# Kernel optimization log

Hardware: AMD Instinct MI355X
Metric: run time of the kernel (lower is better)

## Reference

```python
import jax, jax.numpy as jnp
import numpy as np

EMB = 1024
HEADS = 16
HEAD_DIM = EMB // HEADS


def setup_inputs() -> dict:
    key = jax.random.key(0)
    ks = jax.random.split(key, 5)
    x = jax.random.normal(ks[0], (4, 2048, EMB), dtype=jnp.float32)
    # qkv Linear: weight [3*EMB, EMB] in torch; store transposed for x @ W
    Wqkv = jax.random.normal(ks[1], (EMB, 3 * EMB), dtype=jnp.float32) * (1.0 / np.sqrt(EMB))
    bqkv = jax.random.normal(ks[2], (3 * EMB,), dtype=jnp.float32) * 0.01
    Wout = jax.random.normal(ks[3], (EMB, EMB), dtype=jnp.float32) * (1.0 / np.sqrt(EMB))
    bout = jax.random.normal(ks[4], (EMB,), dtype=jnp.float32) * 0.01
    return {"x": x, "Wqkv": Wqkv, "bqkv": bqkv, "Wout": Wout, "bout": bout}


def reference(x, Wqkv, bqkv, Wout, bout):
    B, N, _ = x.shape
    qkv = x @ Wqkv + bqkv                              # [B, N, 3*EMB]
    qkv = qkv.reshape(B, N, 3, HEADS, HEAD_DIM)
    q, k, v = jnp.moveaxis(qkv, 2, 0)                  # each [B, N, H, D]
    q = jnp.swapaxes(q, 1, 2)                          # [B, H, N, D]
    k = jnp.swapaxes(k, 1, 2)
    v = jnp.swapaxes(v, 1, 2)
    scale = 1.0 / np.sqrt(HEAD_DIM).astype(np.float32)
    scores = jnp.einsum('bhqd,bhkd->bhqk', q, k) * scale
    attn = jax.nn.softmax(scores, axis=-1)             # dropout p=0 (eval)
    out = jnp.einsum('bhqk,bhkd->bhqd', attn, v)       # [B, H, N, D]
    out = jnp.swapaxes(out, 1, 2).reshape(B, N, EMB)
    return out @ Wout + bout
```

## Files before the change

kernel.cpp:

```cpp
#include <hip/hip_runtime.h>

#define SEQ   2048
#define EMBD  1024
#define HEADS 16
#define HDIM  64
#define MTOT  8192
#define LOG2E 1.44269504f

typedef __attribute__((ext_vector_type(8))) _Float16 half8;
typedef __attribute__((ext_vector_type(4))) _Float16 half4;
typedef __attribute__((ext_vector_type(2))) __fp16 fp16x2;
typedef __attribute__((ext_vector_type(4))) float f32x4;

__device__ __forceinline__ f32x4 mfma16(half8 a, half8 b, f32x4 c) {
  return __builtin_amdgcn_mfma_f32_16x16x32_f16(a, b, c, 0, 0, 0);
}

__device__ __forceinline__ void gload_lds16(const void* g, void* l) {
  __builtin_amdgcn_global_load_lds(
      (const __attribute__((address_space(1))) unsigned int*)g,
      (__attribute__((address_space(3))) unsigned int*)l, 16, 0, 0);
}

__global__ void k_cvt(const float* __restrict__ in, _Float16* __restrict__ out) {
  size_t i = (size_t)blockIdx.x * blockDim.x + threadIdx.x;
  const f32x4* in4 = (const f32x4*)in;
  f32x4 a = in4[2 * i], b = in4[2 * i + 1];
  half8 h;
  h[0] = (_Float16)a[0]; h[1] = (_Float16)a[1];
  h[2] = (_Float16)a[2]; h[3] = (_Float16)a[3];
  h[4] = (_Float16)b[0]; h[5] = (_Float16)b[1];
  h[6] = (_Float16)b[2]; h[7] = (_Float16)b[3];
  *(half8*)(out + i * 8) = h;
}

__global__ __launch_bounds__(256) void k_transpose(const float* __restrict__ in,
                                                   _Float16* __restrict__ out,
                                                   int R, int C) {
  __shared__ _Float16 tile[64][65];
  const int tid = threadIdx.x;
  const int r0 = blockIdx.y * 64, c0 = blockIdx.x * 64;
  const int tr = tid >> 6;
  const int tc = tid & 63;
  #pragma unroll
  for (int i = 0; i < 16; ++i) {
    const int r = i * 4 + tr;
    tile[r][tc] = (_Float16)in[(size_t)(r0 + r) * C + c0 + tc];
  }
  __syncthreads();
  #pragma unroll
  for (int i = 0; i < 16; ++i) {
    const int cc = i * 4 + tr;
    out[(size_t)(c0 + cc) * R + r0 + tc] = tile[tc][cc];
  }
}

template<int EPI>
__global__ __launch_bounds__(256) void k_gemm(
    const _Float16* __restrict__ A, const _Float16* __restrict__ Bt,
    const float* __restrict__ bias, float* __restrict__ outf,
    _Float16* __restrict__ q, _Float16* __restrict__ k, _Float16* __restrict__ vt)
{
  __shared__ _Float16 sm[2 * 128 * 64];
  _Float16* sA = sm;
  _Float16* sB = sm + 128 * 64;
  const int tid = threadIdx.x;
  const int l = tid & 63, g = l >> 4, c = l & 15;
  const int w = tid >> 6;
  const int wm = (w >> 1) * 64, wn = (w & 1) * 64;
  const int rowBase = blockIdx.y * 128;
  const int colBase = blockIdx.x * 128;

  f32x4 acc[4][4] = {};

  const _Float16* Ag = A + (size_t)(rowBase + (tid >> 3)) * 1024 + (tid & 7) * 8;
  const _Float16* Bg = Bt + (size_t)(colBase + (tid >> 3)) * 1024 + (tid & 7) * 8;
  _Float16* la = sA + tid * 8;
  _Float16* lb = sB + tid * 8;

  for (int kt = 0; kt < 16; ++kt) {
    const _Float16* ag = Ag + kt * 64;
    const _Float16* bg = Bg + kt * 64;
    #pragma unroll
    for (int i = 0; i < 4; ++i) {
      gload_lds16(ag + (size_t)i * 32 * 1024, la + i * 256 * 8);
      gload_lds16(bg + (size_t)i * 32 * 1024, lb + i * 256 * 8);
    }
    __syncthreads();
    #pragma unroll
    for (int kk = 0; kk < 2; ++kk) {
      half8 af[4], bf[4];
      #pragma unroll
      for (int t = 0; t < 4; ++t)
        af[t] = *(const half8*)(sA + (wm + t * 16 + c) * 64 + kk * 32 + g * 8);
      #pragma unroll
      for (int t = 0; t < 4; ++t)
        bf[t] = *(const half8*)(sB + (wn + t * 16 + c) * 64 + kk * 32 + g * 8);
      #pragma unroll
      for (int mt = 0; mt < 4; ++mt)
        #pragma unroll
        for (int nt = 0; nt < 4; ++nt)
          acc[mt][nt] = mfma16(af[mt], bf[nt], acc[mt][nt]);
    }
    __syncthreads();
  }

  #pragma unroll
  for (int mt = 0; mt < 4; ++mt) {
    #pragma unroll
    for (int nt = 0; nt < 4; ++nt) {
      const int col = colBase + wn + nt * 16 + c;
      const float bv = bias[col];
      #pragma unroll
      for (int r = 0; r < 4; ++r) {
        const int row = rowBase + wm + mt * 16 + g * 4 + r;
        const float val = acc[mt][nt][r] + bv;
        if constexpr (EPI == 0) {
          const int s = col >> 10, h = (col >> 6) & 15, d = col & 63;
          const int b = row >> 11, n = row & 2047;
          const int bh = b * HEADS + h;
          const _Float16 hv = (_Float16)val;
          if (s == 2)      vt[((size_t)bh * HDIM + d) * SEQ + n] = hv;
          else if (s == 1) k [((size_t)bh * SEQ + n) * HDIM + d] = hv;
          else             q [((size_t)bh * SEQ + n) * HDIM + d] = hv;
        } else {
          outf[(size_t)row * EMBD + col] = val;
        }
      }
    }
  }
}

__global__ __launch_bounds__(512) void k_attn(
    const _Float16* __restrict__ q, const _Float16* __restrict__ kg,
    const _Float16* __restrict__ vt, _Float16* __restrict__ aout)
{
  __shared__ _Float16 sm[(64 + 64 + 8 * 32) * 72];
  _Float16* Ks = sm;
  _Float16* Vs = sm + 64 * 72;
  const int tid = threadIdx.x;
  const int w = tid >> 6, l = tid & 63, g = l >> 4, c = l & 15;
  _Float16* Pw = sm + 2 * 64 * 72 + w * 32 * 72;

  const int orig = blockIdx.x;
  const int lb = (orig & 7) * 64 + (orig >> 3);
  const int bh = lb >> 3;
  const int n0 = (lb & 7) * 256 + w * 32;

  const _Float16* qb = q  + (size_t)bh * SEQ * HDIM;
  const _Float16* kb = kg + (size_t)bh * SEQ * HDIM;
  const _Float16* vb = vt + (size_t)bh * HDIM * SEQ;
  const int row0 = tid >> 3, cb = tid & 7;

  half8 aq[2][2];
  #pragma unroll
  for (int qt = 0; qt < 2; ++qt)
    #pragma unroll
    for (int kk = 0; kk < 2; ++kk) {
      half8 t = *(const half8*)(qb + (size_t)(n0 + qt * 16 + c) * HDIM + kk * 32 + g * 8);
      aq[qt][kk] = t * (_Float16)0.125f;
    }

  float m_[2] = {-1e30f, -1e30f};
  float l_[2] = {0.f, 0.f};
  f32x4 o[2][4] = {};

  half8 kr = *(const half8*)(kb + (size_t)tid * 8);
  half8 vr = *(const half8*)(vb + (size_t)row0 * SEQ + cb * 8);

  for (int kt = 0; kt < SEQ / 64; ++kt) {
    __syncthreads();
    *(half8*)(Ks + row0 * 72 + cb * 8) = kr;
    *(half8*)(Vs + row0 * 72 + cb * 8) = vr;
    if (kt + 1 < SEQ / 64) {
      kr = *(const half8*)(kb + (size_t)(kt + 1) * 64 * HDIM + (size_t)tid * 8);
      vr = *(const half8*)(vb + (size_t)row0 * SEQ + (kt + 1) * 64 + cb * 8);
    }
    __syncthreads();

    f32x4 s[4][2] = {};
    __builtin_amdgcn_s_setprio(1);
    #pragma unroll
    for (int kk = 0; kk < 2; ++kk) {
      #pragma unroll
      for (int kt4 = 0; kt4 < 4; ++kt4) {
        half8 ak = *(const half8*)(Ks + (kt4 * 16 + c) * 72 + kk * 32 + g * 8);
        s[kt4][0] = mfma16(ak, aq[0][kk], s[kt4][0]);
        s[kt4][1] = mfma16(ak, aq[1][kk], s[kt4][1]);
      }
    }
    __builtin_amdgcn_s_setprio(0);

    #pragma unroll
    for (int qf = 0; qf < 2; ++qf) {
      float mx = s[0][qf][0];
      #pragma unroll
      for (int kt4 = 0; kt4 < 4; ++kt4)
        #pragma unroll
        for (int r = 0; r < 4; ++r)
          mx = fmaxf(mx, s[kt4][qf][r]);

      if (__any(mx > m_[qf] + 8.0f)) {
        float fm = fmaxf(mx, __shfl_xor(mx, 16, 64));
        fm = fmaxf(fm, __shfl_xor(fm, 32, 64));
        const float mo = m_[qf];
        const float mn = fmaxf(mo, fm);
        const float cor = __builtin_amdgcn_exp2f((mo - mn) * LOG2E);
        m_[qf] = mn;
        l_[qf] *= cor;
        #pragma unroll
        for (int r = 0; r < 4; ++r) {
          const float corr = __shfl(cor, g * 4 + r, 64);
          #pragma unroll
          for (int dt = 0; dt < 4; ++dt)
            o[qf][dt][r] *= corr;
        }
      }
      const float mn = m_[qf];

      float rs = 0.f;
      _Float16* prow = Pw + (qf * 16 + c) * 72;
      #pragma unroll
      for (int kt4 = 0; kt4 < 4; ++kt4) {
        float p0 = __builtin_amdgcn_exp2f((s[kt4][qf][0] - mn) * LOG2E);
        float p1 = __builtin_amdgcn_exp2f((s[kt4][qf][1] - mn) * LOG2E);
        float p2 = __builtin_amdgcn_exp2f((s[kt4][qf][2] - mn) * LOG2E);
        float p3 = __builtin_amdgcn_exp2f((s[kt4][qf][3] - mn) * LOG2E);
        rs += (p0 + p1) + (p2 + p3);
        union { fp16x2 v2[2]; half4 v4; } u;
        u.v2[0] = __builtin_amdgcn_cvt_pkrtz(p0, p1);
        u.v2[1] = __builtin_amdgcn_cvt_pkrtz(p2, p3);
        *(half4*)(prow + kt4 * 16 + g * 4) = u.v4;
      }
      l_[qf] += rs;
    }

    __builtin_amdgcn_s_setprio(1);
    #pragma unroll
    for (int kk = 0; kk < 2; ++kk) {
      half8 ap0 = *(const half8*)(Pw + (0  + c) * 72 + kk * 32 + g * 8);
      half8 ap1 = *(const half8*)(Pw + (16 + c) * 72 + kk * 32 + g * 8);
      #pragma unroll
      for (int dt = 0; dt < 4; ++dt) {
        half8 bv = *(const half8*)(Vs + (dt * 16 + c) * 72 + kk * 32 + g * 8);
        o[0][dt] = mfma16(ap0, bv, o[0][dt]);
        o[1][dt] = mfma16(ap1, bv, o[1][dt]);
      }
    }
    __builtin_amdgcn_s_setprio(0);
  }

  const int b = bh >> 4, h = bh & 15;
  #pragma unroll
  for (int qt = 0; qt < 2; ++qt) {
    float lt = l_[qt];
    lt += __shfl_xor(lt, 16, 64);
    lt += __shfl_xor(lt, 32, 64);
    #pragma unroll
    for (int r = 0; r < 4; ++r) {
      const float lr = __shfl(lt, g * 4 + r, 64);
      const float rl = __builtin_amdgcn_rcpf(lr);
      const int n = n0 + qt * 16 + g * 4 + r;
      #pragma unroll
      for (int dt = 0; dt < 4; ++dt) {
        aout[((size_t)(b * SEQ + n)) * EMBD + h * HDIM + dt * 16 + c] =
            (_Float16)(o[qt][dt][r] * rl);
      }
    }
  }
}

extern "C" void kernel_launch(void* const* d_in, const int* in_sizes, int n_in,
                              void* d_out, int out_size, void* d_ws, size_t ws_size,
                              hipStream_t stream) {
  const float* x    = (const float*)d_in[0];
  const float* Wqkv = (const float*)d_in[1];
  const float* bqkv = (const float*)d_in[2];
  const float* Wout = (const float*)d_in[3];
  const float* bout = (const float*)d_in[4];
  float* out = (float*)d_out;

  _Float16* ws    = (_Float16*)d_ws;
  _Float16* xh    = ws;
  _Float16* wqkvt = xh + (size_t)MTOT * EMBD;
  _Float16* woutt = wqkvt + (size_t)3 * EMBD * EMBD;
  _Float16* qbuf  = woutt + (size_t)EMBD * EMBD;
  _Float16* kbuf  = qbuf + (size_t)MTOT * EMBD;
  _Float16* vtbuf = kbuf + (size_t)MTOT * EMBD;
  _Float16* aout  = xh;

  k_cvt<<<4096, 256, 0, stream>>>(x, xh);
  k_transpose<<<dim3(48, 16), 256, 0, stream>>>(Wqkv, wqkvt, 1024, 3072);
  k_transpose<<<dim3(16, 16), 256, 0, stream>>>(Wout, woutt, 1024, 1024);
  k_gemm<0><<<dim3(24, 64), 256, 0, stream>>>(xh, wqkvt, bqkv, nullptr,
                                              qbuf, kbuf, vtbuf);
  k_attn<<<512, 512, 0, stream>>>(qbuf, kbuf, vtbuf, aout);
  k_gemm<1><<<dim3(8, 64), 256, 0, stream>>>(aout, woutt, bout, out,
                                             nullptr, nullptr, nullptr);
}
```

Before: 242.1 us.

## Switch attention kernel to 32x32x16 MFMA with per-lane query row softmax

The attention kernel moves from 16x16x32 to 32x32x16 MFMA tiles, computing S^T so that each lane owns one query row. Row max and row sum then need only one cross-lane shuffle, and the per-row correction shuffles go away. The output is staged through LDS so each lane writes a full 16-byte vector to global memory, and launch bounds now request 4 blocks per CU with a padded P stride. The risk is higher register pressure from the 16-wide accumulators, which could spill or lower occupancy.

```diff
diff --git a/kernel.cpp b/kernel.cpp
--- a/kernel.cpp
+++ b/kernel.cpp
@@ -11,15 +11,25 @@
 typedef __attribute__((ext_vector_type(4))) _Float16 half4;
 typedef __attribute__((ext_vector_type(2))) __fp16 fp16x2;
 typedef __attribute__((ext_vector_type(4))) float f32x4;
+typedef __attribute__((ext_vector_type(16))) float f32x16;
 
 __device__ __forceinline__ f32x4 mfma16(half8 a, half8 b, f32x4 c) {
   return __builtin_amdgcn_mfma_f32_16x16x32_f16(a, b, c, 0, 0, 0);
+}
+__device__ __forceinline__ f32x16 mfma32(half8 a, half8 b, f32x16 c) {
+  return __builtin_amdgcn_mfma_f32_32x32x16_f16(a, b, c, 0, 0, 0);
 }
 
 __device__ __forceinline__ void gload_lds16(const void* g, void* l) {
   __builtin_amdgcn_global_load_lds(
       (const __attribute__((address_space(1))) unsigned int*)g,
       (__attribute__((address_space(3))) unsigned int*)l, 16, 0, 0);
+}
+
+__device__ __forceinline__ unsigned pk2(float a, float b) {
+  union { fp16x2 v; unsigned u; } t;
+  t.v = __builtin_amdgcn_cvt_pkrtz(a, b);
+  return t.u;
 }
 
 __global__ void k_cvt(const float* __restrict__ in, _Float16* __restrict__ out) {
@@ -131,16 +141,17 @@
   }
 }
 
-__global__ __launch_bounds__(512) void k_attn(
+__global__ __launch_bounds__(512, 4) void k_attn(
     const _Float16* __restrict__ q, const _Float16* __restrict__ kg,
     const _Float16* __restrict__ vt, _Float16* __restrict__ aout)
 {
-  __shared__ _Float16 sm[(64 + 64 + 8 * 32) * 72];
+  __shared__ _Float16 sm[64 * 72 * 2 + 8 * 32 * 76];
   _Float16* Ks = sm;
   _Float16* Vs = sm + 64 * 72;
   const int tid = threadIdx.x;
-  const int w = tid >> 6, l = tid & 63, g = l >> 4, c = l & 15;
-  _Float16* Pw = sm + 2 * 64 * 72 + w * 32 * 72;
+  const int w = tid >> 6, l = tid & 63;
+  const int q32 = l & 31, hi = l >> 5;
+  _Float16* Pw = sm + 2 * 64 * 72 + w * 32 * 76;
 
   const int orig = blockIdx.x;
   const int lb = (orig & 7) * 64 + (orig >> 3);
@@ -152,18 +163,15 @@
   const _Float16* vb = vt + (size_t)bh * HDIM * SEQ;
   const int row0 = tid >> 3, cb = tid & 7;
 
-  half8 aq[2][2];
-  #pragma unroll
-  for (int qt = 0; qt < 2; ++qt)
-    #pragma unroll
-    for (int kk = 0; kk < 2; ++kk) {
-      half8 t = *(const half8*)(qb + (size_t)(n0 + qt * 16 + c) * HDIM + kk * 32 + g * 8);
-      aq[qt][kk] = t * (_Float16)0.125f;
-    }
-
-  float m_[2] = {-1e30f, -1e30f};
-  float l_[2] = {0.f, 0.f};
-  f32x4 o[2][4] = {};
+  half8 aq[4];
+  #pragma unroll
+  for (int ch = 0; ch < 4; ++ch) {
+    half8 t = *(const half8*)(qb + (size_t)(n0 + q32) * HDIM + ch * 16 + hi * 8);
+    aq[ch] = t * (_Float16)0.125f;
+  }
+
+  float m_ = -1e30f, l_ = 0.f;
+  f32x16 o0 = {}, o1 = {};
 
   half8 kr = *(const half8*)(kb + (size_t)tid * 8);
   half8 vr = *(const half8*)(vb + (size_t)row0 * SEQ + cb * 8);
@@ -178,95 +186,91 @@
     }
     __syncthreads();
 
-    f32x4 s[4][2] = {};
+    f32x16 s0 = {}, s1 = {};
     __builtin_amdgcn_s_setprio(1);
     #pragma unroll
-    for (int kk = 0; kk < 2; ++kk) {
-      #pragma unroll
-      for (int kt4 = 0; kt4 < 4; ++kt4) {
-        half8 ak = *(const half8*)(Ks + (kt4 * 16 + c) * 72 + kk * 32 + g * 8);
-        s[kt4][0] = mfma16(ak, aq[0][kk], s[kt4][0]);
-        s[kt4][1] = mfma16(ak, aq[1][kk], s[kt4][1]);
+    for (int ch = 0; ch < 4; ++ch) {
+      half8 ak0 = *(const half8*)(Ks + q32 * 72 + ch * 16 + hi * 8);
+      half8 ak1 = *(const half8*)(Ks + (32 + q32) * 72 + ch * 16 + hi * 8);
+      s0 = mfma32(ak0, aq[ch], s0);
+      s1 = mfma32(ak1, aq[ch], s1);
+    }
+    __builtin_amdgcn_s_setprio(0);
+
+    float mx = fmaxf(s0[0], s1[0]);
+    #pragma unroll
+    for (int e = 1; e < 16; ++e) mx = fmaxf(mx, fmaxf(s0[e], s1[e]));
+
+    if (__any(mx > m_ + 8.0f)) {
+      const float fm = fmaxf(mx, __shfl_xor(mx, 32, 64));
+      const float mo = m_;
+      const float mn = fmaxf(mo, fm);
+      const float cor = __builtin_amdgcn_exp2f((mo - mn) * LOG2E);
+      m_ = mn;
+      l_ *= cor;
+      #pragma unroll
+      for (int e = 0; e < 16; ++e) { o0[e] *= cor; o1[e] *= cor; }
+    }
+
+    float rs = 0.f;
+    #pragma unroll
+    for (int e = 0; e < 16; ++e) {
+      s0[e] = __builtin_amdgcn_exp2f((s0[e] - m_) * LOG2E);
+      s1[e] = __builtin_amdgcn_exp2f((s1[e] - m_) * LOG2E);
+      rs += s0[e] + s1[e];
+    }
+    l_ += rs;
+
+    _Float16* prow = Pw + q32 * 76;
+    #pragma unroll
+    for (int j = 0; j < 4; ++j) {
+      union { unsigned u[2]; half4 h; } t0, t1;
+      t0.u[0] = pk2(s0[4 * j], s0[4 * j + 1]);
+      t0.u[1] = pk2(s0[4 * j + 2], s0[4 * j + 3]);
+      t1.u[0] = pk2(s1[4 * j], s1[4 * j + 1]);
+      t1.u[1] = pk2(s1[4 * j + 2], s1[4 * j + 3]);
+      *(half4*)(prow + 8 * j + 4 * hi) = t0.h;
+      *(half4*)(prow + 32 + 8 * j + 4 * hi) = t1.h;
+    }
+
+    __builtin_amdgcn_s_setprio(1);
+    #pragma unroll
+    for (int ch = 0; ch < 4; ++ch) {
+      half8 pf  = *(const half8*)(Pw + q32 * 76 + ch * 16 + hi * 8);
+      half8 av0 = *(const half8*)(Vs + q32 * 72 + ch * 16 + hi * 8);
+      half8 av1 = *(const half8*)(Vs + (32 + q32) * 72 + ch * 16 + hi * 8);
+      o0 = mfma32(av0, pf, o0);
+      o1 = mfma32(av1, pf, o1);
+    }
+    __builtin_amdgcn_s_setprio(0);
+  }
+
+  float lt = l_ + __shfl_xor(l_, 32, 64);
+  const float rl = __builtin_amdgcn_rcpf(lt);
+
+  _Float16* Ot = Pw;
+  #pragma unroll
+  for (int dh = 0; dh < 2; ++dh) {
+    #pragma unroll
+    for (int j = 0; j < 4; ++j) {
+      union { unsigned u[2]; half4 h; } t;
+      if (dh == 0) {
+        t.u[0] = pk2(o0[4 * j] * rl, o0[4 * j + 1] * rl);
+        t.u[1] = pk2(o0[4 * j + 2] * rl, o0[4 * j + 3] * rl);
+      } else {
+        t.u[0] = pk2(o1[4 * j] * rl, o1[4 * j + 1] * rl);
+        t.u[1] = pk2(o1[4 * j + 2] * rl, o1[4 * j + 3] * rl);
       }
-    }
-    __builtin_amdgcn_s_setprio(0);
-
-    #pragma unroll
-    for (int qf = 0; qf < 2; ++qf) {
-      float mx = s[0][qf][0];
-      #pragma unroll
-      for (int kt4 = 0; kt4 < 4; ++kt4)
-        #pragma unroll
-        for (int r = 0; r < 4; ++r)
-          mx = fmaxf(mx, s[kt4][qf][r]);
-
-      if (__any(mx > m_[qf] + 8.0f)) {
-        float fm = fmaxf(mx, __shfl_xor(mx, 16, 64));
-        fm = fmaxf(fm, __shfl_xor(fm, 32, 64));
-        const float mo = m_[qf];
-        const float mn = fmaxf(mo, fm);
-        const float cor = __builtin_amdgcn_exp2f((mo - mn) * LOG2E);
-        m_[qf] = mn;
-        l_[qf] *= cor;
-        #pragma unroll
-        for (int r = 0; r < 4; ++r) {
-          const float corr = __shfl(cor, g * 4 + r, 64);
-          #pragma unroll
-          for (int dt = 0; dt < 4; ++dt)
-            o[qf][dt][r] *= corr;
-        }
-      }
-      const float mn = m_[qf];
-
-      float rs = 0.f;
-      _Float16* prow = Pw + (qf * 16 + c) * 72;
-      #pragma unroll
-      for (int kt4 = 0; kt4 < 4; ++kt4) {
-        float p0 = __builtin_amdgcn_exp2f((s[kt4][qf][0] - mn) * LOG2E);
-        float p1 = __builtin_amdgcn_exp2f((s[kt4][qf][1] - mn) * LOG2E);
-        float p2 = __builtin_amdgcn_exp2f((s[kt4][qf][2] - mn) * LOG2E);
-        float p3 = __builtin_amdgcn_exp2f((s[kt4][qf][3] - mn) * LOG2E);
-        rs += (p0 + p1) + (p2 + p3);
-        union { fp16x2 v2[2]; half4 v4; } u;
-        u.v2[0] = __builtin_amdgcn_cvt_pkrtz(p0, p1);
-        u.v2[1] = __builtin_amdgcn_cvt_pkrtz(p2, p3);
-        *(half4*)(prow + kt4 * 16 + g * 4) = u.v4;
-      }
-      l_[qf] += rs;
-    }
-
-    __builtin_amdgcn_s_setprio(1);
-    #pragma unroll
-    for (int kk = 0; kk < 2; ++kk) {
-      half8 ap0 = *(const half8*)(Pw + (0  + c) * 72 + kk * 32 + g * 8);
-      half8 ap1 = *(const half8*)(Pw + (16 + c) * 72 + kk * 32 + g * 8);
-      #pragma unroll
-      for (int dt = 0; dt < 4; ++dt) {
-        half8 bv = *(const half8*)(Vs + (dt * 16 + c) * 72 + kk * 32 + g * 8);
-        o[0][dt] = mfma16(ap0, bv, o[0][dt]);
-        o[1][dt] = mfma16(ap1, bv, o[1][dt]);
-      }
-    }
-    __builtin_amdgcn_s_setprio(0);
+      *(half4*)(Ot + q32 * 76 + dh * 32 + 8 * j + 4 * hi) = t.h;
+    }
   }
 
   const int b = bh >> 4, h = bh & 15;
   #pragma unroll
-  for (int qt = 0; qt < 2; ++qt) {
-    float lt = l_[qt];
-    lt += __shfl_xor(lt, 16, 64);
-    lt += __shfl_xor(lt, 32, 64);
-    #pragma unroll
-    for (int r = 0; r < 4; ++r) {
-      const float lr = __shfl(lt, g * 4 + r, 64);
-      const float rl = __builtin_amdgcn_rcpf(lr);
-      const int n = n0 + qt * 16 + g * 4 + r;
-      #pragma unroll
-      for (int dt = 0; dt < 4; ++dt) {
-        aout[((size_t)(b * SEQ + n)) * EMBD + h * HDIM + dt * 16 + c] =
-            (_Float16)(o[qt][dt][r] * rl);
-      }
-    }
+  for (int i = 0; i < 4; ++i) {
+    const int qq = 8 * i + (l >> 3);
+    half8 v = *(const half8*)(Ot + qq * 76 + (l & 7) * 8);
+    *(half8*)(aout + (size_t)(b * SEQ + n0 + qq) * EMBD + h * HDIM + (l & 7) * 8) = v;
   }
 }
 
```

After: 247.6 us. 1.02x slower.
